# Optimization experiments

Measured on AMD Instinct MI355X. Metric: run time of the kernel, lower is better.

## Reference

```python
import math
import jax, jax.numpy as jnp
import numpy as np

NUM_HEADS = 8
K_CRITICAL = 0.05
K_SKIP = 0.10


def setup_inputs() -> dict:
    key = jax.random.key(0)
    ks = jax.random.split(key, 10)
    B, T, D = 1, 2048, 512
    s = 1.0 / math.sqrt(D)
    return {
        'x': jax.random.normal(ks[0], (B, T, D), jnp.float32),
        'wq': jax.random.normal(ks[1], (D, D), jnp.float32) * s,
        'bq': jax.random.normal(ks[2], (D,), jnp.float32) * s,
        'wk': jax.random.normal(ks[3], (D, D), jnp.float32) * s,
        'bk': jax.random.normal(ks[4], (D,), jnp.float32) * s,
        'wv': jax.random.normal(ks[5], (D, D), jnp.float32) * s,
        'bv': jax.random.normal(ks[6], (D,), jnp.float32) * s,
        'wo': jax.random.normal(ks[7], (D, D), jnp.float32) * s,
        'bo': jax.random.normal(ks[8], (D,), jnp.float32) * s,
    }


def _phi(t):
    # elu(t) + 1 -> positive feature map for linear attention
    return jax.nn.elu(t) + 1.0


def reference(x, wq, bq, wk, bk, wv, bv, wo, bo):
    B, T, D = x.shape
    H = NUM_HEADS
    hd = D // H

    # projections (torch nn.Linear: y = x @ W.T + b), split heads -> [B,H,T,hd]
    q = (x @ wq.T + bq).reshape(B, T, H, hd).transpose(0, 2, 1, 3)
    k = (x @ wk.T + bk).reshape(B, T, H, hd).transpose(0, 2, 1, 3)
    v = (x @ wv.T + bv).reshape(B, T, H, hd).transpose(0, 2, 1, 3)

    # full attention scores [B,H,T,T]
    scores = jnp.einsum('bhqd,bhkd->bhqk', q, k) / math.sqrt(hd)

    # per-query quantile thresholds (linear interpolation, like torch.quantile)
    crit_th = jnp.quantile(scores, 1.0 - K_CRITICAL, axis=-1, keepdims=True)
    skip_th = jnp.quantile(scores, K_SKIP, axis=-1, keepdims=True)
    crit_mask = scores > crit_th
    skip_mask = scores < skip_th
    marginal_mask = jnp.logical_not(crit_mask | skip_mask)

    # critical path: softmax over top-k_critical entries only
    crit_scores = jnp.where(crit_mask, scores, -jnp.inf)
    crit_attn = jax.nn.softmax(crit_scores, axis=-1)
    crit_attn = jnp.where(skip_mask, 0.0, crit_attn)
    crit_out = jnp.einsum('bhqk,bhkd->bhqd', crit_attn, v)

    # marginal path: causal (cumulative) linear attention
    q_f = _phi(q)
    k_f = _phi(k)
    kv_cum = jnp.cumsum(k_f[..., :, None] * v[..., None, :], axis=2)  # [B,H,T,hd,hd]
    k_cum = jnp.cumsum(k_f, axis=2)                                   # [B,H,T,hd]
    lin_num = jnp.einsum('bhtd,bhtde->bhte', q_f, kv_cum)             # [B,H,T,hd]
    lin_den = jnp.clip(jnp.sum(q_f * k_cum, axis=-1, keepdims=True), 1e-6, None)
    marginal_active = jnp.mean(marginal_mask.astype(scores.dtype), axis=-1, keepdims=True)
    lin_out = (lin_num / lin_den) * marginal_active

    out = (crit_out + lin_out).transpose(0, 2, 1, 3).reshape(B, T, D)
    out = out @ wo.T + bo  # dropout is identity in eval mode
    return out
```

## Files before the change

### kernel.cpp

```cpp
#include <hip/hip_runtime.h>
#include <math.h>

#define T_SEQ 2048
#define D_MODEL 512
#define H_HEADS 8
#define HD 64
#define NCH 32
#define CSZ 64
#define CAP 192

__device__ __forceinline__ unsigned f2k(float f) {
    unsigned u = __float_as_uint(f);
    return (u & 0x80000000u) ? ~u : (u | 0x80000000u);
}
__device__ __forceinline__ float k2f(unsigned k) {
    unsigned u = (k & 0x80000000u) ? (k & 0x7fffffffu) : ~k;
    return __uint_as_float(u);
}

__device__ __forceinline__ void locate_rank(unsigned rr, unsigned e0,
    const unsigned cc[4], int lane, unsigned& sel_bin, unsigned& sel_nb, unsigned& sel_cnt)
{
    unsigned e1 = e0 + cc[0], e2 = e1 + cc[1], e3 = e2 + cc[2];
    int bin = -1; unsigned nb = 0u, ct = 0u;
    if (rr >= e0 && rr < e1)              { bin = lane * 4 + 0; nb = e0; ct = cc[0]; }
    else if (rr >= e1 && rr < e2)         { bin = lane * 4 + 1; nb = e1; ct = cc[1]; }
    else if (rr >= e2 && rr < e3)         { bin = lane * 4 + 2; nb = e2; ct = cc[2]; }
    else if (rr >= e3 && rr < e3 + cc[3]) { bin = lane * 4 + 3; nb = e3; ct = cc[3]; }
    unsigned long long bal = __ballot(bin >= 0);
    int src = __ffsll((unsigned long long)bal) - 1;
    sel_bin = (unsigned)__shfl(bin, src);
    sel_nb  = (unsigned)__shfl((int)nb, src);
    sel_cnt = (unsigned)__shfl((int)ct, src);
}

__global__ __launch_bounds__(256) void proj_qkv_kernel(
    const float* __restrict__ x,
    const float* __restrict__ wq, const float* __restrict__ bq,
    const float* __restrict__ wk, const float* __restrict__ bk,
    const float* __restrict__ wv, const float* __restrict__ bv,
    float* __restrict__ qh, float* __restrict__ kh, float* __restrict__ vh,
    float* __restrict__ qf, float* __restrict__ kf)
{
    const int which = blockIdx.z;
    const float* W    = (which == 0) ? wq : (which == 1) ? wk : wv;
    const float* bias = (which == 0) ? bq : (which == 1) ? bk : bv;
    float* outh = (which == 0) ? qh : (which == 1) ? kh : vh;
    float* outf = (which == 0) ? qf : (which == 1) ? kf : nullptr;

    __shared__ float As[32][68];
    __shared__ float Bs[32][68];
    const int tid = threadIdx.x;
    const int m0 = blockIdx.x * 64;
    const int n0 = blockIdx.y * 64;
    const int rb = (tid >> 4) * 4;
    const int cb = (tid & 15) * 4;

    float acc[4][4] = {};
    for (int k0 = 0; k0 < D_MODEL; k0 += 32) {
        for (int l = 0; l < 2; ++l) {
            int p = tid + l * 256;
            int row = p >> 3;
            int c4 = (p & 7) * 4;
            float4 av = *(const float4*)(x + (size_t)(m0 + row) * D_MODEL + k0 + c4);
            As[c4 + 0][row] = av.x; As[c4 + 1][row] = av.y;
            As[c4 + 2][row] = av.z; As[c4 + 3][row] = av.w;
            float4 wv4 = *(const float4*)(W + (size_t)(n0 + row) * D_MODEL + k0 + c4);
            Bs[c4 + 0][row] = wv4.x; Bs[c4 + 1][row] = wv4.y;
            Bs[c4 + 2][row] = wv4.z; Bs[c4 + 3][row] = wv4.w;
        }
        __syncthreads();
        #pragma unroll
        for (int kk = 0; kk < 32; ++kk) {
            float4 ar = *(const float4*)&As[kk][rb];
            float4 br = *(const float4*)&Bs[kk][cb];
            float arr[4] = {ar.x, ar.y, ar.z, ar.w};
            float brr[4] = {br.x, br.y, br.z, br.w};
            #pragma unroll
            for (int i = 0; i < 4; ++i)
                #pragma unroll
                for (int j = 0; j < 4; ++j)
                    acc[i][j] = fmaf(arr[i], brr[j], acc[i][j]);
        }
        __syncthreads();
    }
    #pragma unroll
    for (int i = 0; i < 4; ++i) {
        int m = m0 + rb + i;
        #pragma unroll
        for (int j = 0; j < 4; ++j) {
            int n = n0 + cb + j;
            float v = acc[i][j] + bias[n];
            int h = n >> 6, d = n & 63;
            size_t idx = ((size_t)(h * T_SEQ) + m) * HD + d;
            outh[idx] = v;
            if (outf) outf[idx] = (v > 0.f) ? (v + 1.f) : expf(v);
        }
    }
}

__global__ __launch_bounds__(256) void out_proj_kernel(
    const float* __restrict__ att, const float* __restrict__ wo,
    const float* __restrict__ bo, float* __restrict__ out)
{
    __shared__ float As[32][68];
    __shared__ float Bs[32][68];
    const int tid = threadIdx.x;
    const int m0 = blockIdx.x * 64;
    const int n0 = blockIdx.y * 64;
    const int rb = (tid >> 4) * 4;
    const int cb = (tid & 15) * 4;

    float acc[4][4] = {};
    for (int k0 = 0; k0 < D_MODEL; k0 += 32) {
        for (int l = 0; l < 2; ++l) {
            int p = tid + l * 256;
            int row = p >> 3;
            int c4 = (p & 7) * 4;
            float4 av = *(const float4*)(att + (size_t)(m0 + row) * D_MODEL + k0 + c4);
            As[c4 + 0][row] = av.x; As[c4 + 1][row] = av.y;
            As[c4 + 2][row] = av.z; As[c4 + 3][row] = av.w;
            float4 wv4 = *(const float4*)(wo + (size_t)(n0 + row) * D_MODEL + k0 + c4);
            Bs[c4 + 0][row] = wv4.x; Bs[c4 + 1][row] = wv4.y;
            Bs[c4 + 2][row] = wv4.z; Bs[c4 + 3][row] = wv4.w;
        }
        __syncthreads();
        #pragma unroll
        for (int kk = 0; kk < 32; ++kk) {
            float4 ar = *(const float4*)&As[kk][rb];
            float4 br = *(const float4*)&Bs[kk][cb];
            float arr[4] = {ar.x, ar.y, ar.z, ar.w};
            float brr[4] = {br.x, br.y, br.z, br.w};
            #pragma unroll
            for (int i = 0; i < 4; ++i)
                #pragma unroll
                for (int j = 0; j < 4; ++j)
                    acc[i][j] = fmaf(arr[i], brr[j], acc[i][j]);
        }
        __syncthreads();
    }
    #pragma unroll
    for (int i = 0; i < 4; ++i) {
        int m = m0 + rb + i;
        #pragma unroll
        for (int j = 0; j < 4; ++j) {
            int n = n0 + cb + j;
            out[(size_t)m * D_MODEL + n] = acc[i][j] + bo[n];
        }
    }
}

__global__ __launch_bounds__(256) void qk_gemm_kernel(
    const float* __restrict__ qh, const float* __restrict__ kh, float* __restrict__ S)
{
    __shared__ float As[64][132];
    __shared__ float Bs[64][68];
    const int tid = threadIdx.x;
    const int n0 = blockIdx.x * 64;
    const int m0 = blockIdx.y * 128;
    const int h  = blockIdx.z;
    const float* qb = qh + (size_t)h * T_SEQ * HD;
    const float* kb = kh + (size_t)h * T_SEQ * HD;

    #pragma unroll
    for (int l = 0; l < 8; ++l) {
        int p = tid + l * 256;
        int row = p >> 4, c4 = (p & 15) * 4;
        float4 a = *(const float4*)(qb + (size_t)(m0 + row) * HD + c4);
        As[c4 + 0][row] = a.x; As[c4 + 1][row] = a.y;
        As[c4 + 2][row] = a.z; As[c4 + 3][row] = a.w;
    }
    #pragma unroll
    for (int l = 0; l < 4; ++l) {
        int p = tid + l * 256;
        int row = p >> 4, c4 = (p & 15) * 4;
        float4 b = *(const float4*)(kb + (size_t)(n0 + row) * HD + c4);
        Bs[c4 + 0][row] = b.x; Bs[c4 + 1][row] = b.y;
        Bs[c4 + 2][row] = b.z; Bs[c4 + 3][row] = b.w;
    }
    __syncthreads();

    const int rb = (tid >> 4) * 8;
    const int cb = (tid & 15) * 4;
    float acc[8][4] = {};
    #pragma unroll 8
    for (int kk = 0; kk < HD; ++kk) {
        float4 a0 = *(const float4*)&As[kk][rb];
        float4 a1 = *(const float4*)&As[kk][rb + 4];
        float4 br = *(const float4*)&Bs[kk][cb];
        float arr[8] = {a0.x, a0.y, a0.z, a0.w, a1.x, a1.y, a1.z, a1.w};
        float brr[4] = {br.x, br.y, br.z, br.w};
        #pragma unroll
        for (int i = 0; i < 8; ++i)
            #pragma unroll
            for (int j = 0; j < 4; ++j)
                acc[i][j] = fmaf(arr[i], brr[j], acc[i][j]);
    }
    #pragma unroll
    for (int i = 0; i < 8; ++i) {
        float4 o;
        o.x = acc[i][0] * 0.125f; o.y = acc[i][1] * 0.125f;
        o.z = acc[i][2] * 0.125f; o.w = acc[i][3] * 0.125f;
        *(float4*)(S + ((size_t)h * T_SEQ + m0 + rb + i) * T_SEQ + n0 + cb) = o;
    }
}

__global__ __launch_bounds__(256) void select_kernel(
    const float* __restrict__ S, float2* __restrict__ clist,
    int* __restrict__ critcnt, float* __restrict__ marg, float* __restrict__ rowinv)
{
    const int h = blockIdx.y;
    const int r = threadIdx.x >> 6;
    const int lane = threadIdx.x & 63;
    const int t = blockIdx.x * 4 + r;
    __shared__ unsigned hists[4][2][256];

    const float* srow = S + ((size_t)h * T_SEQ + t) * T_SEQ;
    unsigned kr[32];
    unsigned mx = 0u;
    #pragma unroll
    for (int u = 0; u < 8; ++u) {
        float4 f = *(const float4*)(srow + (size_t)(lane + u * 64) * 4);
        kr[u * 4 + 0] = f2k(f.x); kr[u * 4 + 1] = f2k(f.y);
        kr[u * 4 + 2] = f2k(f.z); kr[u * 4 + 3] = f2k(f.w);
        mx = max(mx, max(max(kr[u * 4 + 0], kr[u * 4 + 1]), max(kr[u * 4 + 2], kr[u * 4 + 3])));
    }
    #pragma unroll
    for (int off = 32; off > 0; off >>= 1)
        mx = max(mx, (unsigned)__shfl_xor(mx, off));

    const unsigned rankv[2] = {204u, 1944u};
    unsigned pfx[2], base[2] = {0u, 0u};
    bool res[2] = {false, false};
    unsigned rsh[2] = {0u, 0u};

    {
        uint4 z4 = make_uint4(0u, 0u, 0u, 0u);
        uint4* hv = (uint4*)hists[r];
        hv[lane * 2 + 0] = z4; hv[lane * 2 + 1] = z4;
        #pragma unroll
        for (int u = 0; u < 32; ++u)
            atomicAdd(&hists[r][0][kr[u] >> 24], 1u);
        uint4 a = ((const uint4*)hists[r][0])[lane];
        unsigned cc[4] = {a.x, a.y, a.z, a.w};
        unsigned lsum = cc[0] + cc[1] + cc[2] + cc[3];
        unsigned incl = lsum;
        #pragma unroll
        for (int off = 1; off < 64; off <<= 1) {
            unsigned tv = __shfl_up(incl, off);
            if (lane >= off) incl += tv;
        }
        unsigned e0 = incl - lsum;
        #pragma unroll
        for (int g = 0; g < 2; ++g) {
            unsigned bin, nb, ct;
            locate_rank(rankv[g], e0, cc, lane, bin, nb, ct);
            pfx[g] = bin; base[g] = nb;
            if (ct == 1u) { res[g] = true; rsh[g] = 24u; }
        }
    }

    for (int p = 1; p < 4; ++p) {
        if (res[0] && res[1]) break;
        const int sh = 24 - 8 * p;
        const bool a0 = !res[0], a1 = !res[1];
        const bool dup = a0 && a1 && (pfx[0] == pfx[1]);
        uint4 z4 = make_uint4(0u, 0u, 0u, 0u);
        uint4* hv = (uint4*)hists[r];
        hv[lane * 2 + 0] = z4; hv[lane * 2 + 1] = z4;
        #pragma unroll
        for (int u = 0; u < 32; ++u) {
            unsigned k = kr[u];
            unsigned hi = k >> (sh + 8);
            unsigned bin = (k >> sh) & 255u;
            if (a0 && hi == pfx[0]) atomicAdd(&hists[r][0][bin], 1u);
            if (a1 && !dup && hi == pfx[1]) atomicAdd(&hists[r][1][bin], 1u);
        }
        unsigned cc0[4], e00 = 0u;
        if (a0 || dup) {
            uint4 a = ((const uint4*)hists[r][0])[lane];
            cc0[0] = a.x; cc0[1] = a.y; cc0[2] = a.z; cc0[3] = a.w;
            unsigned lsum = cc0[0] + cc0[1] + cc0[2] + cc0[3];
            unsigned incl = lsum;
            #pragma unroll
            for (int off = 1; off < 64; off <<= 1) {
                unsigned tv = __shfl_up(incl, off);
                if (lane >= off) incl += tv;
            }
            e00 = incl - lsum;
        }
        if (a0) {
            unsigned bin, nb, ct;
            locate_rank(rankv[0] - base[0], e00, cc0, lane, bin, nb, ct);
            pfx[0] = (pfx[0] << 8) | bin; base[0] += nb;
            if (ct == 1u && p < 3) { res[0] = true; rsh[0] = (unsigned)sh; }
        }
        if (a1) {
            unsigned bin, nb, ct;
            if (dup) {
                locate_rank(rankv[1] - base[1], e00, cc0, lane, bin, nb, ct);
            } else {
                uint4 b = ((const uint4*)hists[r][1])[lane];
                unsigned cc1[4] = {b.x, b.y, b.z, b.w};
                unsigned lsum = cc1[0] + cc1[1] + cc1[2] + cc1[3];
                unsigned incl = lsum;
                #pragma unroll
                for (int off = 1; off < 64; off <<= 1) {
                    unsigned tv = __shfl_up(incl, off);
                    if (lane >= off) incl += tv;
                }
                unsigned e10 = incl - lsum;
                locate_rank(rankv[1] - base[1], e10, cc1, lane, bin, nb, ct);
            }
            pfx[1] = (pfx[1] << 8) | bin; base[1] += nb;
            if (ct == 1u && p < 3) { res[1] = true; rsh[1] = (unsigned)sh; }
        }
    }

    unsigned kth0, kth1;
    if (res[0] || res[1]) {
        unsigned m0v = 0xffffffffu, m1v = 0xffffffffu;
        #pragma unroll
        for (int u = 0; u < 32; ++u) {
            unsigned k = kr[u];
            if (res[0] && (k >> rsh[0]) == pfx[0]) m0v = min(m0v, k);
            if (res[1] && (k >> rsh[1]) == pfx[1]) m1v = min(m1v, k);
        }
        #pragma unroll
        for (int off = 32; off > 0; off >>= 1) {
            m0v = min(m0v, (unsigned)__shfl_xor(m0v, off));
            m1v = min(m1v, (unsigned)__shfl_xor(m1v, off));
        }
        kth0 = res[0] ? m0v : pfx[0];
        kth1 = res[1] ? m1v : pfx[1];
    } else {
        kth0 = pfx[0]; kth1 = pfx[1];
    }

    unsigned cle0 = 0;
    #pragma unroll
    for (int u = 0; u < 32; ++u)
        if (kr[u] <= kth0) cle0++;
    #pragma unroll
    for (int off = 32; off > 0; off >>= 1)
        cle0 += (unsigned)__shfl_xor(cle0, off);
    const unsigned scnt = (cle0 > 205u) ? base[0] : cle0;
    const float m = k2f(mx);

    float2* lrow = clist + ((size_t)h * T_SEQ + t) * CAP;
    float z = 0.f;
    unsigned bcnt = 0;
    const unsigned long long pm = (lane == 0) ? 0ull : (~0ull >> (64 - lane));
    #pragma unroll
    for (int u8 = 0; u8 < 8; ++u8) {
        #pragma unroll
        for (int q = 0; q < 4; ++q) {
            unsigned k = kr[u8 * 4 + q];
            bool crit = k > kth1;
            unsigned long long bal = __ballot(crit);
            if (crit) {
                float sv = k2f(k);
                float w = __expf(sv - m);
                z += w;
                unsigned pos = bcnt + (unsigned)__popcll(bal & pm);
                if (pos < CAP) {
                    unsigned j = (unsigned)(4 * lane + 256 * u8 + q);
                    lrow[pos] = make_float2(w, __uint_as_float(j));
                }
            }
            bcnt += (unsigned)__popcll(bal);
        }
    }
    #pragma unroll
    for (int off = 32; off > 0; off >>= 1)
        z += __shfl_xor(z, off);
    if (lane == 0) {
        critcnt[(size_t)h * T_SEQ + t] = (int)min(bcnt, (unsigned)CAP);
        unsigned mc = (unsigned)T_SEQ - bcnt - scnt;
        marg[(size_t)h * T_SEQ + t] = (float)mc * (1.f / (float)T_SEQ);
        rowinv[(size_t)h * T_SEQ + t] = (z > 0.f) ? (1.f / z) : 0.f;
    }
}

__global__ __launch_bounds__(256) void wv_gather_kernel(
    const float2* __restrict__ clist, const int* __restrict__ critcnt,
    const float* __restrict__ rowinv, const float* __restrict__ vh, float* __restrict__ att)
{
    const int h = blockIdx.y;
    const int r = threadIdx.x >> 6;
    const int lane = threadIdx.x & 63;
    const int t = blockIdx.x * 4 + r;
    const float* vb = vh + (size_t)h * T_SEQ * HD;
    const float2* lrow = clist + ((size_t)h * T_SEQ + t) * CAP;
    const int cnt = critcnt[(size_t)h * T_SEQ + t];
    const float invz = rowinv[(size_t)h * T_SEQ + t];

    float acc = 0.f;
    int i = 0;
    for (; i + 8 <= cnt; i += 8) {
        float2 e[8];
        #pragma unroll
        for (int q = 0; q < 8; ++q) e[q] = lrow[i + q];
        #pragma unroll
        for (int q = 0; q < 8; ++q) {
            unsigned j = __float_as_uint(e[q].y);
            acc = fmaf(e[q].x, vb[(size_t)j * HD + lane], acc);
        }
    }
    for (; i < cnt; ++i) {
        float2 e = lrow[i];
        unsigned j = __float_as_uint(e.y);
        acc = fmaf(e.x, vb[(size_t)j * HD + lane], acc);
    }
    att[(size_t)t * D_MODEL + h * HD + lane] += acc * invz;
}

__global__ __launch_bounds__(256) void chunk_sums_kernel(
    const float* __restrict__ kf, const float* __restrict__ vh,
    float* __restrict__ Ac, float* __restrict__ bc)
{
    const int c = blockIdx.x, h = blockIdx.y;
    const int tid = threadIdx.x;
    __shared__ float kfl[CSZ][HD];
    __shared__ float vl[CSZ][HD];
    const size_t base = ((size_t)h * T_SEQ + c * CSZ) * HD;

    for (int l = 0; l < 4; ++l) {
        int p = tid + l * 256;
        int row = p >> 4, c4 = (p & 15) * 4;
        *(float4*)&kfl[row][c4] = *(const float4*)(kf + base + (size_t)row * HD + c4);
        *(float4*)&vl[row][c4]  = *(const float4*)(vh + base + (size_t)row * HD + c4);
    }
    __syncthreads();

    const int d = tid >> 2, e0 = (tid & 3) * 16;
    float acc[16] = {};
    for (int u = 0; u < CSZ; ++u) {
        float a = kfl[u][d];
        #pragma unroll
        for (int i = 0; i < 16; ++i) acc[i] = fmaf(a, vl[u][e0 + i], acc[i]);
    }
    float* Adst = Ac + (((size_t)(h * NCH + c) * HD + d) * HD + e0);
    #pragma unroll
    for (int i = 0; i < 16; ++i) Adst[i] = acc[i];

    if (tid < HD) {
        float sum = 0.f;
        for (int u = 0; u < CSZ; ++u) sum += kfl[u][tid];
        bc[(size_t)(h * NCH + c) * HD + tid] = sum;
    }
}

__global__ __launch_bounds__(256) void prefix_kernel(
    const float* __restrict__ Ac, const float* __restrict__ bc,
    float* __restrict__ Sx, float* __restrict__ sx)
{
    const int h = blockIdx.x;
    const int tid = threadIdx.x;
    float run[16];
    #pragma unroll
    for (int i = 0; i < 16; ++i) run[i] = 0.f;
    for (int c = 0; c < NCH; ++c) {
        const float* a = Ac + (size_t)(h * NCH + c) * 4096;
        float* sdst = Sx + (size_t)(h * NCH + c) * 4096;
        #pragma unroll
        for (int i = 0; i < 16; ++i) {
            int idx = tid + i * 256;
            sdst[idx] = run[i];
            run[i] += a[idx];
        }
    }
    if (tid < HD) {
        float rb = 0.f;
        for (int c = 0; c < NCH; ++c) {
            sx[(size_t)(h * NCH + c) * HD + tid] = rb;
            rb += bc[(size_t)(h * NCH + c) * HD + tid];
        }
    }
}

__global__ __launch_bounds__(256) void lin_combine_kernel(
    const float* __restrict__ qf, const float* __restrict__ kf, const float* __restrict__ vh,
    const float* __restrict__ Sx, const float* __restrict__ sx,
    const float* __restrict__ marg, float* __restrict__ att)
{
    const int c = blockIdx.x, h = blockIdx.y;
    const int tid = threadIdx.x;
    __shared__ float Qs[CSZ][65];
    __shared__ float Ks[CSZ][65];
    __shared__ float P[CSZ][66];
    __shared__ float svv[HD];
    __shared__ float coef[CSZ];

    const size_t base = ((size_t)h * T_SEQ + c * CSZ) * HD;
    for (int l = 0; l < 4; ++l) {
        int p = tid + l * 256;
        int row = p >> 4, c4 = (p & 15) * 4;
        *(float4*)&Qs[row][c4] = *(const float4*)(qf + base + (size_t)row * HD + c4);
        *(float4*)&Ks[row][c4] = *(const float4*)(kf + base + (size_t)row * HD + c4);
    }
    if (tid < HD) svv[tid] = sx[(size_t)(h * NCH + c) * HD + tid];
    __syncthreads();

    {
        const int tq = tid >> 2, u0 = (tid & 3) * 16;
        float pr[16];
        #pragma unroll
        for (int i = 0; i < 16; ++i) pr[i] = 0.f;
        for (int d = 0; d < HD; ++d) {
            float qv = Qs[tq][d];
            #pragma unroll
            for (int i = 0; i < 16; ++i) pr[i] = fmaf(qv, Ks[u0 + i][d], pr[i]);
        }
        #pragma unroll
        for (int i = 0; i < 16; ++i) P[tq][u0 + i] = (u0 + i <= tq) ? pr[i] : 0.f;
    }
    __syncthreads();

    if (tid < CSZ) {
        const int tq = tid;
        float den = 0.f;
        for (int d = 0; d < HD; ++d) den += Qs[tq][d] * svv[d];
        for (int u = 0; u <= tq; ++u) den += P[tq][u];
        den = fmaxf(den, 1e-6f);
        coef[tq] = marg[(size_t)h * T_SEQ + c * CSZ + tq] / den;
    }
    {
        const float* Sbase = Sx + (size_t)(h * NCH + c) * 4096;
        for (int l = 0; l < 4; ++l) {
            int p = tid + l * 256;
            int row = p >> 4, c4 = (p & 15) * 4;
            *(float4*)&Ks[row][c4] = *(const float4*)(Sbase + (size_t)row * HD + c4);
        }
    }
    __syncthreads();

    {
        const int tq = tid >> 2, e0 = (tid & 3) * 16;
        float acc[16];
        #pragma unroll
        for (int i = 0; i < 16; ++i) acc[i] = 0.f;
        for (int d = 0; d < HD; ++d) {
            float qv = Qs[tq][d];
            #pragma unroll
            for (int i = 0; i < 16; ++i) acc[i] = fmaf(qv, Ks[d][e0 + i], acc[i]);
        }
        const float* vb = vh + base;
        for (int u = 0; u <= tq; ++u) {
            float pv = P[tq][u];
            #pragma unroll
            for (int i = 0; i < 16; ++i) acc[i] = fmaf(pv, vb[(size_t)u * HD + e0 + i], acc[i]);
        }
        const float cf = coef[tq];
        float* dst = att + (size_t)(c * CSZ + tq) * D_MODEL + h * HD + e0;
        #pragma unroll
        for (int i = 0; i < 16; ++i) dst[i] = acc[i] * cf;
    }
}

extern "C" void kernel_launch(void* const* d_in, const int* in_sizes, int n_in,
                              void* d_out, int out_size, void* d_ws, size_t ws_size,
                              hipStream_t stream)
{
    const float* x  = (const float*)d_in[0];
    const float* wq = (const float*)d_in[1];
    const float* bq = (const float*)d_in[2];
    const float* wk = (const float*)d_in[3];
    const float* bk = (const float*)d_in[4];
    const float* wv = (const float*)d_in[5];
    const float* bv = (const float*)d_in[6];
    const float* wo = (const float*)d_in[7];
    const float* bo = (const float*)d_in[8];
    float* out = (float*)d_out;

    float* ws = (float*)d_ws;
    const size_t NTD = (size_t)T_SEQ * D_MODEL;
    const size_t NSS = (size_t)H_HEADS * T_SEQ * T_SEQ;
    const size_t NROW = (size_t)H_HEADS * T_SEQ;
    float* S    = ws;
    float* qh   = S + NSS;
    float* kh   = qh + NTD;
    float* vh   = kh + NTD;
    float* qf   = vh + NTD;
    float* kf   = qf + NTD;
    float* att  = kf + NTD;
    float* Ac   = att + NTD;
    float* Sx   = Ac + NTD;
    float* bc   = Sx + NTD;
    float* sx   = bc + 16384;
    float* marg = sx + 16384;
    float2* clist = (float2*)(marg + 16384);
    int* critcnt  = (int*)(clist + NROW * CAP);
    float* rowinv = (float*)(critcnt + NROW);

    dim3 b256(256);
    proj_qkv_kernel<<<dim3(32, 8, 3), b256, 0, stream>>>(x, wq, bq, wk, bk, wv, bv,
                                                         qh, kh, vh, qf, kf);
    qk_gemm_kernel<<<dim3(32, 16, 8), b256, 0, stream>>>(qh, kh, S);
    select_kernel<<<dim3(T_SEQ / 4, H_HEADS), b256, 0, stream>>>(S, clist, critcnt, marg, rowinv);
    chunk_sums_kernel<<<dim3(NCH, H_HEADS), b256, 0, stream>>>(kf, vh, Ac, bc);
    prefix_kernel<<<dim3(H_HEADS), b256, 0, stream>>>(Ac, bc, Sx, sx);
    lin_combine_kernel<<<dim3(NCH, H_HEADS), b256, 0, stream>>>(qf, kf, vh, Sx, sx, marg, att);
    wv_gather_kernel<<<dim3(T_SEQ / 4, H_HEADS), b256, 0, stream>>>(clist, critcnt, rowinv, vh, att);
    out_proj_kernel<<<dim3(32, 8), b256, 0, stream>>>(att, wo, bo, out);
}
```

Measured before the change: 321.4 us.

## Fuse critical-path value gather into select kernel via shared-memory list

```diff
diff --git a/kernel.cpp b/kernel.cpp
--- a/kernel.cpp
+++ b/kernel.cpp
@@ -206,8 +206,8 @@
 }
 
 __global__ __launch_bounds__(256) void select_kernel(
-    const float* __restrict__ S, float2* __restrict__ clist,
-    int* __restrict__ critcnt, float* __restrict__ marg, float* __restrict__ rowinv)
+    const float* __restrict__ S, const float* __restrict__ vh,
+    float* __restrict__ att, float* __restrict__ marg)
 {
     const int h = blockIdx.y;
     const int r = threadIdx.x >> 6;
@@ -230,7 +230,7 @@
         mx = max(mx, (unsigned)__shfl_xor(mx, off));
 
     const unsigned rankv[2] = {204u, 1944u};
-    unsigned pfx[2], base[2] = {0u, 0u};
+    unsigned pfx[2], base[2] = {0u, 0u}, fct[2] = {0u, 0u};
     bool res[2] = {false, false};
     unsigned rsh[2] = {0u, 0u};
 
@@ -255,7 +255,7 @@
         for (int g = 0; g < 2; ++g) {
             unsigned bin, nb, ct;
             locate_rank(rankv[g], e0, cc, lane, bin, nb, ct);
-            pfx[g] = bin; base[g] = nb;
+            pfx[g] = bin; base[g] = nb; fct[g] = ct;
             if (ct == 1u) { res[g] = true; rsh[g] = 24u; }
         }
     }
@@ -292,7 +292,7 @@
         if (a0) {
             unsigned bin, nb, ct;
             locate_rank(rankv[0] - base[0], e00, cc0, lane, bin, nb, ct);
-            pfx[0] = (pfx[0] << 8) | bin; base[0] += nb;
+            pfx[0] = (pfx[0] << 8) | bin; base[0] += nb; fct[0] = ct;
             if (ct == 1u && p < 3) { res[0] = true; rsh[0] = (unsigned)sh; }
         }
         if (a1) {
@@ -312,7 +312,7 @@
                 unsigned e10 = incl - lsum;
                 locate_rank(rankv[1] - base[1], e10, cc1, lane, bin, nb, ct);
             }
-            pfx[1] = (pfx[1] << 8) | bin; base[1] += nb;
+            pfx[1] = (pfx[1] << 8) | bin; base[1] += nb; fct[1] = ct;
             if (ct == 1u && p < 3) { res[1] = true; rsh[1] = (unsigned)sh; }
         }
     }
@@ -336,18 +336,13 @@
     } else {
         kth0 = pfx[0]; kth1 = pfx[1];
     }
-
-    unsigned cle0 = 0;
-    #pragma unroll
-    for (int u = 0; u < 32; ++u)
-        if (kr[u] <= kth0) cle0++;
-    #pragma unroll
-    for (int off = 32; off > 0; off >>= 1)
-        cle0 += (unsigned)__shfl_xor(cle0, off);
+    (void)kth0;
+
+    const unsigned cle0 = base[0] + fct[0];
     const unsigned scnt = (cle0 > 205u) ? base[0] : cle0;
     const float m = k2f(mx);
 
-    float2* lrow = clist + ((size_t)h * T_SEQ + t) * CAP;
+    float2* list = (float2*)hists[r];
     float z = 0.f;
     unsigned bcnt = 0;
     const unsigned long long pm = (lane == 0) ? 0ull : (~0ull >> (64 - lane));
@@ -365,7 +360,7 @@
                 unsigned pos = bcnt + (unsigned)__popcll(bal & pm);
                 if (pos < CAP) {
                     unsigned j = (unsigned)(4 * lane + 256 * u8 + q);
-                    lrow[pos] = make_float2(w, __uint_as_float(j));
+                    list[pos] = make_float2(w, __uint_as_float(j));
                 }
             }
             bcnt += (unsigned)__popcll(bal);
@@ -374,45 +369,28 @@
     #pragma unroll
     for (int off = 32; off > 0; off >>= 1)
         z += __shfl_xor(z, off);
+    const float invz = (z > 0.f) ? (1.f / z) : 0.f;
+
+    const float* vb = vh + (size_t)h * T_SEQ * HD;
+    const int cnt = (int)min(bcnt, (unsigned)CAP);
+    float acc = 0.f;
+    int i = 0;
+    for (; i + 4 <= cnt; i += 4) {
+        float2 e0 = list[i], e1 = list[i + 1], e2 = list[i + 2], e3 = list[i + 3];
+        acc = fmaf(e0.x, vb[(size_t)__float_as_uint(e0.y) * HD + lane], acc);
+        acc = fmaf(e1.x, vb[(size_t)__float_as_uint(e1.y) * HD + lane], acc);
+        acc = fmaf(e2.x, vb[(size_t)__float_as_uint(e2.y) * HD + lane], acc);
+        acc = fmaf(e3.x, vb[(size_t)__float_as_uint(e3.y) * HD + lane], acc);
+    }
+    for (; i < cnt; ++i) {
+        float2 e = list[i];
+        acc = fmaf(e.x, vb[(size_t)__float_as_uint(e.y) * HD + lane], acc);
+    }
+    att[(size_t)t * D_MODEL + h * HD + lane] = acc * invz;
     if (lane == 0) {
-        critcnt[(size_t)h * T_SEQ + t] = (int)min(bcnt, (unsigned)CAP);
         unsigned mc = (unsigned)T_SEQ - bcnt - scnt;
         marg[(size_t)h * T_SEQ + t] = (float)mc * (1.f / (float)T_SEQ);
-        rowinv[(size_t)h * T_SEQ + t] = (z > 0.f) ? (1.f / z) : 0.f;
-    }
-}
-
-__global__ __launch_bounds__(256) void wv_gather_kernel(
-    const float2* __restrict__ clist, const int* __restrict__ critcnt,
-    const float* __restrict__ rowinv, const float* __restrict__ vh, float* __restrict__ att)
-{
-    const int h = blockIdx.y;
-    const int r = threadIdx.x >> 6;
-    const int lane = threadIdx.x & 63;
-    const int t = blockIdx.x * 4 + r;
-    const float* vb = vh + (size_t)h * T_SEQ * HD;
-    const float2* lrow = clist + ((size_t)h * T_SEQ + t) * CAP;
-    const int cnt = critcnt[(size_t)h * T_SEQ + t];
-    const float invz = rowinv[(size_t)h * T_SEQ + t];
-
-    float acc = 0.f;
-    int i = 0;
-    for (; i + 8 <= cnt; i += 8) {
-        float2 e[8];
-        #pragma unroll
-        for (int q = 0; q < 8; ++q) e[q] = lrow[i + q];
-        #pragma unroll
-        for (int q = 0; q < 8; ++q) {
-            unsigned j = __float_as_uint(e[q].y);
-            acc = fmaf(e[q].x, vb[(size_t)j * HD + lane], acc);
-        }
-    }
-    for (; i < cnt; ++i) {
-        float2 e = lrow[i];
-        unsigned j = __float_as_uint(e.y);
-        acc = fmaf(e.x, vb[(size_t)j * HD + lane], acc);
-    }
-    att[(size_t)t * D_MODEL + h * HD + lane] += acc * invz;
+    }
 }
 
 __global__ __launch_bounds__(256) void chunk_sums_kernel(
@@ -554,7 +532,7 @@
         const float cf = coef[tq];
         float* dst = att + (size_t)(c * CSZ + tq) * D_MODEL + h * HD + e0;
         #pragma unroll
-        for (int i = 0; i < 16; ++i) dst[i] = acc[i] * cf;
+        for (int i = 0; i < 16; ++i) dst[i] += acc[i] * cf;
     }
 }
 
@@ -576,7 +554,6 @@
     float* ws = (float*)d_ws;
     const size_t NTD = (size_t)T_SEQ * D_MODEL;
     const size_t NSS = (size_t)H_HEADS * T_SEQ * T_SEQ;
-    const size_t NROW = (size_t)H_HEADS * T_SEQ;
     float* S    = ws;
     float* qh   = S + NSS;
     float* kh   = qh + NTD;
@@ -589,18 +566,14 @@
     float* bc   = Sx + NTD;
     float* sx   = bc + 16384;
     float* marg = sx + 16384;
-    float2* clist = (float2*)(marg + 16384);
-    int* critcnt  = (int*)(clist + NROW * CAP);
-    float* rowinv = (float*)(critcnt + NROW);
 
     dim3 b256(256);
     proj_qkv_kernel<<<dim3(32, 8, 3), b256, 0, stream>>>(x, wq, bq, wk, bk, wv, bv,
                                                          qh, kh, vh, qf, kf);
     qk_gemm_kernel<<<dim3(32, 16, 8), b256, 0, stream>>>(qh, kh, S);
-    select_kernel<<<dim3(T_SEQ / 4, H_HEADS), b256, 0, stream>>>(S, clist, critcnt, marg, rowinv);
+    select_kernel<<<dim3(T_SEQ / 4, H_HEADS), b256, 0, stream>>>(S, vh, att, marg);
     chunk_sums_kernel<<<dim3(NCH, H_HEADS), b256, 0, stream>>>(kf, vh, Ac, bc);
     prefix_kernel<<<dim3(H_HEADS), b256, 0, stream>>>(Ac, bc, Sx, sx);
     lin_combine_kernel<<<dim3(NCH, H_HEADS), b256, 0, stream>>>(qf, kf, vh, Sx, sx, marg, att);
-    wv_gather_kernel<<<dim3(T_SEQ / 4, H_HEADS), b256, 0, stream>>>(clist, critcnt, rowinv, vh, att);
     out_proj_kernel<<<dim3(32, 8), b256, 0, stream>>>(att, wo, bo, out);
 }
```

New measurement: 298.2 us. -7.2%, faster.
